# Optimization experiments

Measured on AMD Instinct MI355X. Metric: run time of the kernel, lower is better.

## Reference

```python
import jax, jax.numpy as jnp
import numpy as np

DIM = 192
NUM_HEADS = 6
WINDOW = (2, 6, 12)
INPUT_RES = (8, 48, 180)
TYPE_OF_WINDOWS = (INPUT_RES[0] // WINDOW[0]) * (INPUT_RES[1] // WINDOW[1])  # 32
N_TOK = WINDOW[0] * WINDOW[1] * WINDOW[2]  # 144
NLON = INPUT_RES[2] // WINDOW[2]  # 15
TABLE_ROWS = WINDOW[0] ** 2 * WINDOW[1] ** 2 * (2 * WINDOW[2] - 1)  # 3312


def calculate_position_bias_indices(ws):
    wz, wh, ww = ws
    zi = np.arange(wz)
    zj = -np.arange(wz) * wz
    hi = np.arange(wh)
    hj = -np.arange(wh) * wh
    w = np.arange(ww)
    c1 = np.stack(np.meshgrid(zi, hi, w, indexing='ij')).reshape(3, -1)
    c2 = np.stack(np.meshgrid(zj, hj, w, indexing='ij')).reshape(3, -1)
    coords = (c1[:, :, None] - c2[:, None, :]).transpose(1, 2, 0).copy()
    coords[:, :, 2] += ww - 1
    coords[:, :, 1] *= 2 * ww - 1
    coords[:, :, 0] *= (2 * ww - 1) * wh * wh
    return coords.sum(-1)  # (N, N) in [0, TABLE_ROWS)


def setup_inputs() -> dict:
    key = jax.random.key(0)
    ks = jax.random.split(key, 7)
    B_ = NLON  # batch=1 times nLon window columns
    x = jax.random.normal(ks[0], (B_, TYPE_OF_WINDOWS, N_TOK, DIM), dtype=jnp.float32)
    mask = jax.random.normal(ks[1], (NLON, TYPE_OF_WINDOWS, N_TOK, N_TOK), dtype=jnp.float32)
    qkv_w = jax.random.normal(ks[2], (3 * DIM, DIM), dtype=jnp.float32) * 0.02
    qkv_b = jax.random.normal(ks[3], (3 * DIM,), dtype=jnp.float32) * 0.02
    proj_w = jax.random.normal(ks[4], (DIM, DIM), dtype=jnp.float32) * 0.02
    proj_b = jax.random.normal(ks[5], (DIM,), dtype=jnp.float32) * 0.02
    bias_table = jax.random.normal(ks[6], (TABLE_ROWS, TYPE_OF_WINDOWS, NUM_HEADS), dtype=jnp.float32) * 0.02
    position_index = jnp.asarray(calculate_position_bias_indices(WINDOW), dtype=jnp.int64)
    return {"x": x, "mask": mask, "qkv_w": qkv_w, "qkv_b": qkv_b,
            "proj_w": proj_w, "proj_b": proj_b, "bias_table": bias_table,
            "position_index": position_index}


def reference(x, mask, qkv_w, qkv_b, proj_w, proj_b, bias_table, position_index):
    B_, nW_, N, C = x.shape
    H = NUM_HEADS
    hd = C // H
    scale = hd ** (-0.5)
    # qkv projection: (B_, nW_, N, 3, H, hd)
    qkv = (jnp.einsum('bwnc,dc->bwnd', x, qkv_w) + qkv_b).reshape(B_, nW_, N, 3, H, hd)
    q = qkv[:, :, :, 0] * scale  # (B_, nW_, N, H, hd)
    k = qkv[:, :, :, 1]
    v = qkv[:, :, :, 2]
    # attention scores: (B_, H, nW_, N, N)
    attn = jnp.einsum('bwihd,bwjhd->bhwij', q, k)
    # gathered earth position bias -> (H, nW_, N, N)
    bias = bias_table[position_index.reshape(-1)]  # (N*N, nW_, H)
    bias = bias.reshape(N, N, nW_, H).transpose(3, 2, 0, 1)
    attn = attn + bias[None]
    # mask add: view (B_//nLon, nLon, H, nW_, N, N) + mask (nLon, 1, nW_, N, N)
    nLon = mask.shape[0]
    attn = attn.reshape(B_ // nLon, nLon, H, nW_, N, N) + mask[None, :, None]
    attn = attn.reshape(B_, H, nW_, N, N)
    attn = jax.nn.softmax(attn, axis=-1)
    out = jnp.einsum('bhwij,bwjhd->bwihd', attn, v).reshape(B_, nW_, N, C)
    out = jnp.einsum('bwnc,dc->bwnd', out, proj_w) + proj_b
    return out
```

## Files before the change

kernel.cpp:

```cpp
#include <hip/hip_runtime.h>
#include <hip/hip_bf16.h>

#define B_LON 15
#define NW    32
#define NTOK  144
#define DIM   192
#define NH    6
#define HD    32
#define K3    576
#define MROWS (B_LON*NW*NTOK)
#define NN    (NTOK*NTOK)
#define SCALE 0.17677669529663687f

typedef __attribute__((ext_vector_type(8))) short bf16x8;
typedef __attribute__((ext_vector_type(8))) unsigned short u16x8;
typedef __attribute__((ext_vector_type(4))) float f32x4;

__device__ inline unsigned short f2bf(float f) {
  __bf16 h = (__bf16)f;
  return __builtin_bit_cast(unsigned short, h);
}
__device__ inline float bf2f(unsigned short u) {
  union { unsigned int i; float f; } c;
  c.i = ((unsigned int)u) << 16;
  return c.f;
}

#define NX8 1658880
#define NQ8 13824
#define NP8 4608

__global__ __launch_bounds__(256) void conv_bf_k(
    const float* __restrict__ x, const float* __restrict__ qw,
    const float* __restrict__ pw,
    unsigned short* __restrict__ xbf, unsigned short* __restrict__ qwbf,
    unsigned short* __restrict__ pwbf) {
  const long gid = (long)blockIdx.x * 256 + threadIdx.x;
  const float* src;
  unsigned short* dst;
  long off;
  if (gid < NX8)            { src = x;  dst = xbf;  off = gid; }
  else if (gid < NX8 + NQ8) { src = qw; dst = qwbf; off = gid - NX8; }
  else                      { src = pw; dst = pwbf; off = gid - NX8 - NQ8; }
  const float4 a = ((const float4*)src)[off * 2];
  const float4 b = ((const float4*)src)[off * 2 + 1];
  u16x8 u = {f2bf(a.x), f2bf(a.y), f2bf(a.z), f2bf(a.w),
             f2bf(b.x), f2bf(b.y), f2bf(b.z), f2bf(b.w)};
  *(u16x8*)&dst[off * 8] = u;
}

__global__ __launch_bounds__(256) void bias_pre_k(
    const float* __restrict__ btab, const int* __restrict__ pos,
    unsigned short* __restrict__ biasb) {
  const int wh  = blockIdx.x;
  const int seg = blockIdx.y * 2304;
  unsigned short* dst = biasb + (size_t)wh * NN;
#pragma unroll
  for (int it = 0; it < 9; ++it) {
    const int e = seg + it * 256 + threadIdx.x;
    dst[e] = f2bf(btab[(size_t)pos[e] * (NW * NH) + wh]);
  }
}

__global__ __launch_bounds__(192, 3) void fused_attn_k(
    const unsigned short* __restrict__ X, const unsigned short* __restrict__ W,
    const float* __restrict__ Bv, const float* __restrict__ mask,
    const unsigned short* __restrict__ biasb, unsigned short* __restrict__ ao) {
  __shared__ unsigned short Qs[NTOK * 36];
  __shared__ unsigned short Ks[NTOK * 36];
  __shared__ unsigned short Vs[32 * 160];
  __shared__ unsigned short Ps[3 * 16 * 168];

  const int t    = threadIdx.x;
  const int wave = t / 64;
  const int lane = t & 63;
  const int ln15 = lane & 15;
  const int quad = lane >> 4;
  const int idx  = blockIdx.x;
  const int xcd  = idx & 7;
  const int j0   = idx >> 3;
  const int h    = j0 % 6;
  const int bw   = (j0 / 6) * 8 + xcd;
  const int w    = bw & 31;
  const int wh   = w * NH + h;
  const float* maskp = mask + (size_t)bw * NN;
  const unsigned short* biasp = biasb + (size_t)wh * NN;
  unsigned short* ps = &Ps[wave * 16 * 168];
  const int wv3 = wave * 3;

  if (t < 64) {
    u16x8 z = {0, 0, 0, 0, 0, 0, 0, 0};
    *(u16x8*)&Vs[(t >> 1) * 160 + 144 + (t & 1) * 8] = z;
  }
  {
    ushort4 z = {0, 0, 0, 0};
    *(ushort4*)&ps[(lane >> 2) * 168 + 144 + (lane & 3) * 4] = z;
  }

  f32x4 acc[3][6];
#pragma unroll
  for (int mt = 0; mt < 3; ++mt)
#pragma unroll
    for (int nt = 0; nt < 6; ++nt) acc[mt][nt] = (f32x4){0.f, 0.f, 0.f, 0.f};

#pragma unroll
  for (int kk = 0; kk < 6; ++kk) {
    const int k0 = kk * 32 + quad * 8;
    bf16x8 af[3], bfr[6];
#pragma unroll
    for (int mt = 0; mt < 3; ++mt)
      af[mt] = *(const bf16x8*)&X[(size_t)(bw * NTOK + (wv3 + mt) * 16 + ln15) * DIM + k0];
#pragma unroll
    for (int nt = 0; nt < 6; ++nt) {
      const int wrow = (nt >> 1) * DIM + h * HD + (nt & 1) * 16 + ln15;
      bfr[nt] = *(const bf16x8*)&W[(size_t)wrow * DIM + k0];
    }
#pragma unroll
    for (int mt = 0; mt < 3; ++mt)
#pragma unroll
      for (int nt = 0; nt < 6; ++nt)
        acc[mt][nt] = __builtin_amdgcn_mfma_f32_16x16x32_bf16(
            af[mt], bfr[nt], acc[mt][nt], 0, 0, 0);
  }

#pragma unroll
  for (int nt = 0; nt < 6; ++nt) {
    const int dd   = (nt & 1) * 16 + ln15;
    const float bias = Bv[(nt >> 1) * DIM + h * HD + dd];
#pragma unroll
    for (int mt = 0; mt < 3; ++mt) {
      const int tok = (wv3 + mt) * 16 + quad * 4;
#pragma unroll
      for (int r = 0; r < 4; ++r) {
        const float v = acc[mt][nt][r] + bias;
        if (nt < 2)      Qs[(tok + r) * 36 + dd] = f2bf(v * SCALE);
        else if (nt < 4) Ks[(tok + r) * 36 + dd] = f2bf(v);
        else             Vs[dd * 160 + tok + r]  = f2bf(v);
      }
    }
  }
  __syncthreads();

  for (int g = wv3; g < wv3 + 3; ++g) {
    const int i0 = g * 16;
    const int ib = i0 + quad * 4;

    const bf16x8 qf = *(const bf16x8*)&Qs[(i0 + ln15) * 36 + quad * 8];
    f32x4 s[9];
#pragma unroll
    for (int jt = 0; jt < 9; ++jt) {
      const bf16x8 kf = *(const bf16x8*)&Ks[(jt * 16 + ln15) * 36 + quad * 8];
      s[jt] = (f32x4){0.f, 0.f, 0.f, 0.f};
      s[jt] = __builtin_amdgcn_mfma_f32_16x16x32_bf16(qf, kf, s[jt], 0, 0, 0);
    }

#pragma unroll
    for (int jt = 0; jt < 9; ++jt) {
      const int j = jt * 16 + ln15;
#pragma unroll
      for (int r = 0; r < 4; ++r) {
        const int ij = (ib + r) * NTOK + j;
        s[jt][r] += bf2f(biasp[ij]) + maskp[ij];
      }
    }

    float rinv[4];
#pragma unroll
    for (int r = 0; r < 4; ++r) {
      float mx = s[0][r];
#pragma unroll
      for (int jt = 1; jt < 9; ++jt) mx = fmaxf(mx, s[jt][r]);
#pragma unroll
      for (int off = 1; off < 16; off <<= 1) mx = fmaxf(mx, __shfl_xor(mx, off));
      float sum = 0.f;
#pragma unroll
      for (int jt = 0; jt < 9; ++jt) {
        const float e = __expf(s[jt][r] - mx);
        s[jt][r] = e;
        sum += e;
      }
#pragma unroll
      for (int off = 1; off < 16; off <<= 1) sum += __shfl_xor(sum, off);
      rinv[r] = 1.0f / sum;
    }

#pragma unroll
    for (int jt = 0; jt < 9; ++jt)
#pragma unroll
      for (int r = 0; r < 4; ++r)
        ps[(quad * 4 + r) * 168 + jt * 16 + ln15] = f2bf(s[jt][r]);

    f32x4 o[2] = {{0.f, 0.f, 0.f, 0.f}, {0.f, 0.f, 0.f, 0.f}};
#pragma unroll
    for (int kt = 0; kt < 5; ++kt) {
      const bf16x8 pf = *(const bf16x8*)&ps[ln15 * 168 + kt * 32 + quad * 8];
#pragma unroll
      for (int nt = 0; nt < 2; ++nt) {
        const bf16x8 vf = *(const bf16x8*)&Vs[(nt * 16 + ln15) * 160 + kt * 32 + quad * 8];
        o[nt] = __builtin_amdgcn_mfma_f32_16x16x32_bf16(pf, vf, o[nt], 0, 0, 0);
      }
    }

#pragma unroll
    for (int nt = 0; nt < 2; ++nt)
#pragma unroll
      for (int r = 0; r < 4; ++r)
        ao[(size_t)(bw * NTOK + ib + r) * DIM + h * HD + nt * 16 + ln15] =
            f2bf(o[nt][r] * rinv[r]);
  }
}

__global__ __launch_bounds__(256) void proj_gemm_k(
    const unsigned short* __restrict__ AO, const unsigned short* __restrict__ W,
    const float* __restrict__ Bv, float* __restrict__ out) {
  __shared__ unsigned short As[128 * 200];
  __shared__ unsigned short Bs[64 * 200];
  const int t    = threadIdx.x;
  const int n0   = blockIdx.x * 64;
  const int m0   = blockIdx.y * 128;
  const int w    = t >> 6;
  const int lane = t & 63;
  const int ln15 = lane & 15;
  const int quad = lane >> 4;

#pragma unroll
  for (int it = t; it < 3072; it += 256) {
    const int row = it / 24;
    const int c8  = (it % 24) * 8;
    *(u16x8*)&As[row * 200 + c8] = *(const u16x8*)&AO[(size_t)(m0 + row) * 192 + c8];
  }
#pragma unroll
  for (int it = t; it < 1536; it += 256) {
    const int row = it / 24;
    const int c8  = (it % 24) * 8;
    *(u16x8*)&Bs[row * 200 + c8] = *(const u16x8*)&W[(size_t)(n0 + row) * 192 + c8];
  }
  __syncthreads();

  f32x4 acc[2][4];
#pragma unroll
  for (int i = 0; i < 2; ++i)
#pragma unroll
    for (int jj = 0; jj < 4; ++jj) acc[i][jj] = (f32x4){0.f, 0.f, 0.f, 0.f};

#pragma unroll
  for (int k0 = 0; k0 < 192; k0 += 32) {
    bf16x8 af[2], bfr[4];
#pragma unroll
    for (int mt = 0; mt < 2; ++mt)
      af[mt] = *(bf16x8*)&As[(w * 32 + mt * 16 + ln15) * 200 + k0 + quad * 8];
#pragma unroll
    for (int nt = 0; nt < 4; ++nt)
      bfr[nt] = *(bf16x8*)&Bs[(nt * 16 + ln15) * 200 + k0 + quad * 8];
#pragma unroll
    for (int mt = 0; mt < 2; ++mt)
#pragma unroll
      for (int nt = 0; nt < 4; ++nt)
        acc[mt][nt] = __builtin_amdgcn_mfma_f32_16x16x32_bf16(
            af[mt], bfr[nt], acc[mt][nt], 0, 0, 0);
  }

#pragma unroll
  for (int nt = 0; nt < 4; ++nt) {
    const int colg = n0 + nt * 16 + ln15;
    const float bias = Bv[colg];
#pragma unroll
    for (int mt = 0; mt < 2; ++mt) {
#pragma unroll
      for (int r = 0; r < 4; ++r) {
        const int m = m0 + w * 32 + mt * 16 + quad * 4 + r;
        out[(size_t)m * 192 + colg] = acc[mt][nt][r] + bias;
      }
    }
  }
}

extern "C" void kernel_launch(void* const* d_in, const int* in_sizes, int n_in,
                              void* d_out, int out_size, void* d_ws, size_t ws_size,
                              hipStream_t stream) {
  const float* x      = (const float*)d_in[0];
  const float* mask   = (const float*)d_in[1];
  const float* qkv_w  = (const float*)d_in[2];
  const float* qkv_b  = (const float*)d_in[3];
  const float* proj_w = (const float*)d_in[4];
  const float* proj_b = (const float*)d_in[5];
  const float* btab   = (const float*)d_in[6];
  const int*   pos    = (const int*)d_in[7];
  float* out = (float*)d_out;

  unsigned short* ws = (unsigned short*)d_ws;
  const size_t sz = (size_t)MROWS * DIM;
  unsigned short* aobuf = ws;
  unsigned short* biasb = ws + sz + 256;
  unsigned short* xbf   = biasb + (size_t)192 * NN + 256;
  unsigned short* qwbf  = xbf + sz;
  unsigned short* pwbf  = qwbf + (size_t)K3 * DIM;

  conv_bf_k<<<NX8 / 256 + NQ8 / 256 + NP8 / 256, 256, 0, stream>>>(
      x, qkv_w, proj_w, xbf, qwbf, pwbf);
  bias_pre_k<<<dim3(NW * NH, 9), 256, 0, stream>>>(btab, pos, biasb);
  fused_attn_k<<<NH * 480, 192, 0, stream>>>(
      xbf, qwbf, qkv_b, mask, biasb, aobuf);
  proj_gemm_k<<<dim3(DIM / 64, MROWS / 128), 256, 0, stream>>>(
      aobuf, pwbf, proj_b, out);
}
```

Before: 281.6 us.

## Fuse x bf16 conversion into attention kernel and prefetch mask/bias tiles

The separate pass that converts the whole x tensor to bf16 is removed. The attention kernel now reads fp32 x directly and converts it in registers while loading the QKV GEMM operands, which avoids writing and re-reading a bf16 copy of x. Mask and bias values for the next 16-row group are also loaded into registers before the barrier and during softmax, so their global latency overlaps with compute. The costs are that x is re-read in fp32 by each of the six head blocks, and the prefetch arrays add register pressure under the 3-blocks-per-SM launch bound.

```diff
diff --git a/kernel.cpp b/kernel.cpp
--- a/kernel.cpp
+++ b/kernel.cpp
@@ -25,23 +25,26 @@
   c.i = ((unsigned int)u) << 16;
   return c.f;
 }
-
-#define NX8 1658880
+__device__ inline bf16x8 ldx8(const float* __restrict__ p) {
+  const float4 a = *(const float4*)p;
+  const float4 b = *(const float4*)(p + 4);
+  u16x8 u = {f2bf(a.x), f2bf(a.y), f2bf(a.z), f2bf(a.w),
+             f2bf(b.x), f2bf(b.y), f2bf(b.z), f2bf(b.w)};
+  return __builtin_bit_cast(bf16x8, u);
+}
+
 #define NQ8 13824
 #define NP8 4608
 
 __global__ __launch_bounds__(256) void conv_bf_k(
-    const float* __restrict__ x, const float* __restrict__ qw,
-    const float* __restrict__ pw,
-    unsigned short* __restrict__ xbf, unsigned short* __restrict__ qwbf,
-    unsigned short* __restrict__ pwbf) {
+    const float* __restrict__ qw, const float* __restrict__ pw,
+    unsigned short* __restrict__ qwbf, unsigned short* __restrict__ pwbf) {
   const long gid = (long)blockIdx.x * 256 + threadIdx.x;
   const float* src;
   unsigned short* dst;
   long off;
-  if (gid < NX8)            { src = x;  dst = xbf;  off = gid; }
-  else if (gid < NX8 + NQ8) { src = qw; dst = qwbf; off = gid - NX8; }
-  else                      { src = pw; dst = pwbf; off = gid - NX8 - NQ8; }
+  if (gid < NQ8) { src = qw; dst = qwbf; off = gid; }
+  else           { src = pw; dst = pwbf; off = gid - NQ8; }
   const float4 a = ((const float4*)src)[off * 2];
   const float4 b = ((const float4*)src)[off * 2 + 1];
   u16x8 u = {f2bf(a.x), f2bf(a.y), f2bf(a.z), f2bf(a.w),
@@ -62,8 +65,23 @@
   }
 }
 
+__device__ __forceinline__ void issue_bm(
+    const float* __restrict__ maskp, const unsigned short* __restrict__ biasp,
+    int ibase, int ln15, float fm[9][4], unsigned short fb[9][4]) {
+#pragma unroll
+  for (int jt = 0; jt < 9; ++jt) {
+    const int j = jt * 16 + ln15;
+#pragma unroll
+    for (int r = 0; r < 4; ++r) {
+      const int ij = (ibase + r) * NTOK + j;
+      fm[jt][r] = maskp[ij];
+      fb[jt][r] = biasp[ij];
+    }
+  }
+}
+
 __global__ __launch_bounds__(192, 3) void fused_attn_k(
-    const unsigned short* __restrict__ X, const unsigned short* __restrict__ W,
+    const float* __restrict__ X, const unsigned short* __restrict__ W,
     const float* __restrict__ Bv, const float* __restrict__ mask,
     const unsigned short* __restrict__ biasb, unsigned short* __restrict__ ao) {
   __shared__ unsigned short Qs[NTOK * 36];
@@ -109,7 +127,7 @@
     bf16x8 af[3], bfr[6];
 #pragma unroll
     for (int mt = 0; mt < 3; ++mt)
-      af[mt] = *(const bf16x8*)&X[(size_t)(bw * NTOK + (wv3 + mt) * 16 + ln15) * DIM + k0];
+      af[mt] = ldx8(&X[(size_t)(bw * NTOK + (wv3 + mt) * 16 + ln15) * DIM + k0]);
 #pragma unroll
     for (int nt = 0; nt < 6; ++nt) {
       const int wrow = (nt >> 1) * DIM + h * HD + (nt & 1) * 16 + ln15;
@@ -139,9 +157,16 @@
       }
     }
   }
+
+  float fm[9][4];
+  unsigned short fb[9][4];
+  issue_bm(maskp, biasp, wv3 * 16 + quad * 4, ln15, fm, fb);
+
   __syncthreads();
 
-  for (int g = wv3; g < wv3 + 3; ++g) {
+#pragma unroll
+  for (int gi = 0; gi < 3; ++gi) {
+    const int g  = wv3 + gi;
     const int i0 = g * 16;
     const int ib = i0 + quad * 4;
 
@@ -155,14 +180,13 @@
     }
 
 #pragma unroll
-    for (int jt = 0; jt < 9; ++jt) {
-      const int j = jt * 16 + ln15;
-#pragma unroll
-      for (int r = 0; r < 4; ++r) {
-        const int ij = (ib + r) * NTOK + j;
-        s[jt][r] += bf2f(biasp[ij]) + maskp[ij];
-      }
-    }
+    for (int jt = 0; jt < 9; ++jt)
+#pragma unroll
+      for (int r = 0; r < 4; ++r)
+        s[jt][r] += bf2f(fb[jt][r]) + fm[jt][r];
+
+    if (gi < 2)
+      issue_bm(maskp, biasp, (g + 1) * 16 + quad * 4, ln15, fm, fb);
 
     float rinv[4];
 #pragma unroll
@@ -292,15 +316,13 @@
   const size_t sz = (size_t)MROWS * DIM;
   unsigned short* aobuf = ws;
   unsigned short* biasb = ws + sz + 256;
-  unsigned short* xbf   = biasb + (size_t)192 * NN + 256;
-  unsigned short* qwbf  = xbf + sz;
+  unsigned short* qwbf  = biasb + (size_t)192 * NN + 256;
   unsigned short* pwbf  = qwbf + (size_t)K3 * DIM;
 
-  conv_bf_k<<<NX8 / 256 + NQ8 / 256 + NP8 / 256, 256, 0, stream>>>(
-      x, qkv_w, proj_w, xbf, qwbf, pwbf);
+  conv_bf_k<<<(NQ8 + NP8) / 256, 256, 0, stream>>>(qkv_w, proj_w, qwbf, pwbf);
   bias_pre_k<<<dim3(NW * NH, 9), 256, 0, stream>>>(btab, pos, biasb);
   fused_attn_k<<<NH * 480, 192, 0, stream>>>(
-      xbf, qwbf, qkv_b, mask, biasb, aobuf);
+      x, qwbf, qkv_b, mask, biasb, aobuf);
   proj_gemm_k<<<dim3(DIM / 64, MROWS / 128), 256, 0, stream>>>(
       aobuf, pwbf, proj_b, out);
 }
```

Result: no change. 283.2 us (+0.6%).

## Transpose score MFMA for row-contiguous mask loads and stage bias column in LDS

Applied to the files above, without the earlier changes.

The QK^T MFMA operands are swapped so each lane holds four consecutive key columns of one query row. Mask and bias can then be read as float4/ushort4 vectors, the softmax reductions need only two cross-lane shuffles, and normalized probabilities are packed into LDS with vector stores. Separately, the bias precompute kernel first stages one table column in shared memory and then gathers from it, using fewer blocks. The strided mask read on the hot path becomes coalesced-per-lane vector loads, in exchange for more work per bias block.

```diff
diff --git a/kernel.cpp b/kernel.cpp
--- a/kernel.cpp
+++ b/kernel.cpp
@@ -10,6 +10,7 @@
 #define K3    576
 #define MROWS (B_LON*NW*NTOK)
 #define NN    (NTOK*NTOK)
+#define TROWS 3312
 #define SCALE 0.17677669529663687f
 
 typedef __attribute__((ext_vector_type(8))) short bf16x8;
@@ -52,13 +53,18 @@
 __global__ __launch_bounds__(256) void bias_pre_k(
     const float* __restrict__ btab, const int* __restrict__ pos,
     unsigned short* __restrict__ biasb) {
-  const int wh  = blockIdx.x;
-  const int seg = blockIdx.y * 2304;
+  __shared__ float col[TROWS];
+  const int wh = blockIdx.x;
+  const int t  = threadIdx.x;
+  for (int i = t; i < TROWS; i += 256)
+    col[i] = btab[(size_t)i * (NW * NH) + wh];
+  __syncthreads();
   unsigned short* dst = biasb + (size_t)wh * NN;
-#pragma unroll
-  for (int it = 0; it < 9; ++it) {
-    const int e = seg + it * 256 + threadIdx.x;
-    dst[e] = f2bf(btab[(size_t)pos[e] * (NW * NH) + wh]);
+  const int seg = blockIdx.y * 6912;
+#pragma unroll
+  for (int it = 0; it < 27; ++it) {
+    const int e = seg + it * 256 + t;
+    dst[e] = f2bf(col[pos[e]]);
   }
 }
 
@@ -143,7 +149,7 @@
 
   for (int g = wv3; g < wv3 + 3; ++g) {
     const int i0 = g * 16;
-    const int ib = i0 + quad * 4;
+    const int irow = i0 + ln15;
 
     const bf16x8 qf = *(const bf16x8*)&Qs[(i0 + ln15) * 36 + quad * 8];
     f32x4 s[9];
@@ -151,44 +157,46 @@
     for (int jt = 0; jt < 9; ++jt) {
       const bf16x8 kf = *(const bf16x8*)&Ks[(jt * 16 + ln15) * 36 + quad * 8];
       s[jt] = (f32x4){0.f, 0.f, 0.f, 0.f};
-      s[jt] = __builtin_amdgcn_mfma_f32_16x16x32_bf16(qf, kf, s[jt], 0, 0, 0);
+      s[jt] = __builtin_amdgcn_mfma_f32_16x16x32_bf16(kf, qf, s[jt], 0, 0, 0);
     }
 
 #pragma unroll
     for (int jt = 0; jt < 9; ++jt) {
-      const int j = jt * 16 + ln15;
+      const int jb = jt * 16 + quad * 4;
+      const float4  m4 = *(const float4*)&maskp[(size_t)irow * NTOK + jb];
+      const ushort4 b4 = *(const ushort4*)&biasp[(size_t)irow * NTOK + jb];
+      s[jt][0] += bf2f(b4.x) + m4.x;
+      s[jt][1] += bf2f(b4.y) + m4.y;
+      s[jt][2] += bf2f(b4.z) + m4.z;
+      s[jt][3] += bf2f(b4.w) + m4.w;
+    }
+
+    float mx = s[0][0];
+#pragma unroll
+    for (int jt = 0; jt < 9; ++jt)
+#pragma unroll
+      for (int r = 0; r < 4; ++r) mx = fmaxf(mx, s[jt][r]);
+    mx = fmaxf(mx, __shfl_xor(mx, 16));
+    mx = fmaxf(mx, __shfl_xor(mx, 32));
+    float sum = 0.f;
+#pragma unroll
+    for (int jt = 0; jt < 9; ++jt)
 #pragma unroll
       for (int r = 0; r < 4; ++r) {
-        const int ij = (ib + r) * NTOK + j;
-        s[jt][r] += bf2f(biasp[ij]) + maskp[ij];
-      }
-    }
-
-    float rinv[4];
-#pragma unroll
-    for (int r = 0; r < 4; ++r) {
-      float mx = s[0][r];
-#pragma unroll
-      for (int jt = 1; jt < 9; ++jt) mx = fmaxf(mx, s[jt][r]);
-#pragma unroll
-      for (int off = 1; off < 16; off <<= 1) mx = fmaxf(mx, __shfl_xor(mx, off));
-      float sum = 0.f;
-#pragma unroll
-      for (int jt = 0; jt < 9; ++jt) {
         const float e = __expf(s[jt][r] - mx);
         s[jt][r] = e;
         sum += e;
       }
-#pragma unroll
-      for (int off = 1; off < 16; off <<= 1) sum += __shfl_xor(sum, off);
-      rinv[r] = 1.0f / sum;
-    }
-
-#pragma unroll
-    for (int jt = 0; jt < 9; ++jt)
-#pragma unroll
-      for (int r = 0; r < 4; ++r)
-        ps[(quad * 4 + r) * 168 + jt * 16 + ln15] = f2bf(s[jt][r]);
+    sum += __shfl_xor(sum, 16);
+    sum += __shfl_xor(sum, 32);
+    const float rinv = 1.0f / sum;
+
+#pragma unroll
+    for (int jt = 0; jt < 9; ++jt) {
+      ushort4 pw = {f2bf(s[jt][0] * rinv), f2bf(s[jt][1] * rinv),
+                    f2bf(s[jt][2] * rinv), f2bf(s[jt][3] * rinv)};
+      *(ushort4*)&ps[ln15 * 168 + jt * 16 + quad * 4] = pw;
+    }
 
     f32x4 o[2] = {{0.f, 0.f, 0.f, 0.f}, {0.f, 0.f, 0.f, 0.f}};
 #pragma unroll
@@ -201,12 +209,13 @@
       }
     }
 
+    const int ib = i0 + quad * 4;
 #pragma unroll
     for (int nt = 0; nt < 2; ++nt)
 #pragma unroll
       for (int r = 0; r < 4; ++r)
         ao[(size_t)(bw * NTOK + ib + r) * DIM + h * HD + nt * 16 + ln15] =
-            f2bf(o[nt][r] * rinv[r]);
+            f2bf(o[nt][r]);
   }
 }
 
@@ -298,7 +307,7 @@
 
   conv_bf_k<<<NX8 / 256 + NQ8 / 256 + NP8 / 256, 256, 0, stream>>>(
       x, qkv_w, proj_w, xbf, qwbf, pwbf);
-  bias_pre_k<<<dim3(NW * NH, 9), 256, 0, stream>>>(btab, pos, biasb);
+  bias_pre_k<<<dim3(NW * NH, 3), 256, 0, stream>>>(btab, pos, biasb);
   fused_attn_k<<<NH * 480, 192, 0, stream>>>(
       xbf, qwbf, qkv_b, mask, biasb, aobuf);
   proj_gemm_k<<<dim3(DIM / 64, MROWS / 128), 256, 0, stream>>>(
```

New measurement: 308.0 us. 1.09x slower.
